# Kernel optimization log

Measured on AMD Instinct MI355X. Metric: run time of the kernel, lower is better.

Reference implementation:

```python
import jax, jax.numpy as jnp
import numpy as np

B, N, IN_C, HID, K1, K2, OUT_C = 128, 512, 128, 32, 100, 10, 10
E_PER = 8192  # edges per graph (avg degree 16)
EPS = 1e-15


def _lin(key, fan_in, fan_out):
    return jax.random.normal(key, (fan_in, fan_out), jnp.float32) / np.sqrt(fan_in)


def setup_inputs() -> dict:
    key = jax.random.key(0)
    ks = jax.random.split(key, 20)
    total = B * N
    x = jax.random.normal(ks[0], (total, IN_C), jnp.float32)
    # per-graph random edges, offset into the global node index space
    src_l = jax.random.randint(ks[1], (B, E_PER), 0, N)
    dst_l = jax.random.randint(ks[2], (B, E_PER), 0, N)
    off = (jnp.arange(B, dtype=jnp.int32) * N)[:, None]
    edge_index = jnp.stack([(src_l + off).reshape(-1), (dst_l + off).reshape(-1)]).astype(jnp.int32)
    batch = (jnp.arange(total, dtype=jnp.int32) // N).astype(jnp.int32)
    return {
        "x": x,
        "edge_index": edge_index,
        "batch": batch,
        "conv1_W": _lin(ks[3], IN_C, HID), "conv1_b": jnp.zeros((HID,), jnp.float32),
        "pool1_W": _lin(ks[4], HID, K1), "pool1_b": jnp.zeros((K1,), jnp.float32),
        "conv2_rel_W": _lin(ks[5], HID, HID), "conv2_rel_b": jnp.zeros((HID,), jnp.float32),
        "conv2_root_W": _lin(ks[6], HID, HID),
        "pool2_W": _lin(ks[7], HID, K2), "pool2_b": jnp.zeros((K2,), jnp.float32),
        "conv3_rel_W": _lin(ks[8], HID, HID), "conv3_rel_b": jnp.zeros((HID,), jnp.float32),
        "conv3_root_W": _lin(ks[9], HID, HID),
        "lin1_W": _lin(ks[10], HID, HID), "lin1_b": jnp.zeros((HID,), jnp.float32),
        "lin2_W": _lin(ks[11], HID, OUT_C), "lin2_b": jnp.zeros((OUT_C,), jnp.float32),
    }


def gcn_conv(x, edge_index, W, b):
    # GCNConv with add_self_loops=True, symmetric normalization
    total = x.shape[0]
    loops = jnp.arange(total, dtype=edge_index.dtype)
    src = jnp.concatenate([edge_index[0], loops])
    dst = jnp.concatenate([edge_index[1], loops])
    w = jnp.ones(src.shape[0], x.dtype)
    deg = jax.ops.segment_sum(w, dst, num_segments=total)
    dis = jnp.where(deg > 0, jax.lax.rsqrt(deg), 0.0)
    norm = dis[src] * dis[dst]
    xw = x @ W
    out = jax.ops.segment_sum(norm[:, None] * xw[src], dst, num_segments=total)
    return out + b


def dense_mincut_pool(x, adj, s, mask=None):
    # x:[b,n,f] adj:[b,n,n] s:[b,n,k]
    s = jax.nn.softmax(s, axis=-1)
    if mask is not None:
        m = mask[..., None].astype(x.dtype)
        x = x * m
        s = s * m
    out = jnp.einsum('bnk,bnf->bkf', s, x)
    out_adj = jnp.einsum('bnk,bnm,bml->bkl', s, adj, s)
    mincut_num = jnp.trace(out_adj, axis1=-2, axis2=-1)
    d_flat = adj.sum(-1)  # [b,n]
    mincut_den = jnp.einsum('bnk,bn,bnk->b', s, d_flat, s)  # trace(s^T D s)
    mincut_loss = jnp.mean(-(mincut_num / mincut_den))
    k = s.shape[-1]
    ss = jnp.einsum('bnk,bnl->bkl', s, s)
    ss_norm = jnp.linalg.norm(ss, axis=(-1, -2), keepdims=True)
    i_s = jnp.eye(k, dtype=x.dtype) / jnp.sqrt(jnp.asarray(k, x.dtype))  # I_k / ||I_k||_F
    ortho_loss = jnp.mean(jnp.linalg.norm(ss / ss_norm - i_s, axis=(-1, -2)))
    # zero diagonal then symmetric degree-normalize
    out_adj = out_adj * (1.0 - jnp.eye(k, dtype=x.dtype))
    d = jnp.sqrt(out_adj.sum(-1))[..., None] + EPS
    out_adj = out_adj / d / jnp.swapaxes(d, -1, -2)
    return out, out_adj, mincut_loss, ortho_loss


def dense_graph_conv(x, adj, rel_W, rel_b, root_W):
    # DenseGraphConv(aggr='add'): lin_rel(adj @ x) + lin_root(x)
    return (adj @ x) @ rel_W + rel_b + x @ root_W


def reference(x, edge_index, batch, conv1_W, conv1_b, pool1_W, pool1_b,
              conv2_rel_W, conv2_rel_b, conv2_root_W, pool2_W, pool2_b,
              conv3_rel_W, conv3_rel_b, conv3_root_W, lin1_W, lin1_b, lin2_W, lin2_b):
    h = jax.nn.relu(gcn_conv(x, edge_index, conv1_W, conv1_b))
    # to_dense_batch: sorted batch with N nodes per graph -> reshape; mask all-true
    xd = h.reshape(B, N, HID)
    mask = jnp.ones((B, N), bool)
    # to_dense_adj
    b_idx = edge_index[0] // N
    s_l = edge_index[0] % N
    d_l = edge_index[1] % N
    adj = jnp.zeros((B, N, N), x.dtype).at[b_idx, s_l, d_l].add(1.0)
    s = xd @ pool1_W + pool1_b
    xd, adj, mc1, o1 = dense_mincut_pool(xd, adj, s, mask)
    xd = jax.nn.relu(dense_graph_conv(xd, adj, conv2_rel_W, conv2_rel_b, conv2_root_W))
    s = xd @ pool2_W + pool2_b
    xd, adj, mc2, o2 = dense_mincut_pool(xd, adj, s)
    xd = dense_graph_conv(xd, adj, conv3_rel_W, conv3_rel_b, conv3_root_W)
    g = xd.mean(axis=1)  # [B, HID]
    g = jax.nn.relu(g @ lin1_W + lin1_b)
    g = g @ lin2_W + lin2_b
    return jax.nn.log_softmax(g, axis=-1), mc1 + mc2 + o1 + o2
```

## Files before the change

kernel.cpp:

```cpp
#include <hip/hip_runtime.h>
#include <hip/hip_bf16.h>

#define TB   128
#define NN   512
#define INC  128
#define HH   32
#define KP1  100
#define KP2  10
#define OC   10
#define EPER 8192
#define NT   (TB*NN)
#define ET   (TB*EPER)
#define ZTR  264
#define ZTS  40
#define XTS  136

typedef unsigned int  u32;
typedef unsigned short u16;
typedef __attribute__((ext_vector_type(8))) short bf16x8;
typedef __attribute__((ext_vector_type(16))) float f32x16;

__device__ __forceinline__ u32 bfr(float f) {
    u32 b = __float_as_uint(f);
    return (b + 0x7fffu + ((b >> 16) & 1u)) >> 16;
}
__device__ __forceinline__ u32 pk2(float a, float b) { return bfr(a) | (bfr(b) << 16); }
__device__ __forceinline__ float blo(u32 u) { return __uint_as_float(u << 16); }
__device__ __forceinline__ float bhi(u32 u) { return __uint_as_float(u & 0xffff0000u); }

__global__ __launch_bounds__(1024) void k_sort(const int* __restrict__ ei,
                                               int* __restrict__ cnt_src, int* __restrict__ cnt_dst,
                                               int* __restrict__ off_src, int* __restrict__ off_dst,
                                               u16* __restrict__ srt_dst, u16* __restrict__ srt_src,
                                               float* __restrict__ dis, float* __restrict__ aux) {
    __shared__ int hs[NN], hd[NN], ps[NN], pd[NN];
    __shared__ __align__(16) u16 sdl[EPER], ssl[EPER];
    int g = blockIdx.x, tid = threadIdx.x, goff = g * NN;
    if (tid == 0) aux[g] = 0.f;
    if (tid < NN) { hs[tid] = 0; hd[tid] = 0; }
    __syncthreads();
    const int* es = ei + (size_t)g * EPER;
    const int* ed = ei + ET + (size_t)g * EPER;
    for (int e = tid; e < EPER; e += 1024) {
        atomicAdd(&hs[es[e] - goff], 1);
        atomicAdd(&hd[ed[e] - goff], 1);
    }
    __syncthreads();
    int vs = 0, vd = 0;
    if (tid < NN) { vs = hs[tid]; vd = hd[tid]; ps[tid] = vs; pd[tid] = vd; }
    __syncthreads();
    for (int off = 1; off < NN; off <<= 1) {
        int xa = 0, xb = 0;
        if (tid < NN) {
            xa = ps[tid]; xb = pd[tid];
            if (tid >= off) { xa += ps[tid - off]; xb += pd[tid - off]; }
        }
        __syncthreads();
        if (tid < NN) { ps[tid] = xa; pd[tid] = xb; }
        __syncthreads();
    }
    int eso = 0, edo = 0;
    if (tid < NN) {
        eso = ps[tid] - vs; edo = pd[tid] - vd;
        cnt_src[goff + tid] = vs;  cnt_dst[goff + tid] = vd;
        off_src[goff + tid] = g * EPER + eso;
        off_dst[goff + tid] = g * EPER + edo;
        dis[goff + tid] = rsqrtf(1.0f + (float)vd);
    }
    __syncthreads();
    if (tid < NN) { ps[tid] = eso; pd[tid] = edo; }
    __syncthreads();
    for (int e = tid; e < EPER; e += 1024) {
        int s = es[e] - goff, d = ed[e] - goff;
        int p = atomicAdd(&ps[s], 1); sdl[p] = (u16)d;
        int q = atomicAdd(&pd[d], 1); ssl[q] = (u16)s;
    }
    __syncthreads();
    u32* wd = (u32*)(srt_dst + (size_t)g * EPER);
    u32* ws = (u32*)(srt_src + (size_t)g * EPER);
    const u32* rd = (const u32*)sdl;
    const u32* rs = (const u32*)ssl;
    for (int i = tid; i < EPER / 2; i += 1024) { wd[i] = rd[i]; ws[i] = rs[i]; }
}

__global__ __launch_bounds__(256) void k_xw2(const float* __restrict__ x, const float* __restrict__ W,
                                             u16* __restrict__ xwb) {
    __shared__ u16 sX[128 * XTS];
    __shared__ u16 sW[32 * XTS];
    int tid = threadIdx.x;
    int nbase = blockIdx.x * 128;
    for (int i = tid; i < INC * HH; i += 256) {
        int k = i >> 5, n = i & 31;
        sW[n * XTS + k] = (u16)bfr(W[i]);
    }
    for (int i = tid; i < 128 * 32; i += 256) {
        int r = i >> 5, q = i & 31;
        float4 v = ((const float4*)(x + (size_t)(nbase + r) * INC))[q];
        u32* dst = (u32*)&sX[r * XTS + q * 4];
        dst[0] = pk2(v.x, v.y);
        dst[1] = pk2(v.z, v.w);
    }
    __syncthreads();
    int wave = tid >> 6, lane = tid & 63;
    int lc = lane & 31, half = lane >> 5;
    f32x16 acc;
#pragma unroll
    for (int r = 0; r < 16; r++) acc[r] = 0.f;
#pragma unroll
    for (int kc = 0; kc < 8; kc++) {
        bf16x8 af  = *(const bf16x8*)&sX[(wave * 32 + lc) * XTS + kc * 16 + half * 8];
        bf16x8 bfv = *(const bf16x8*)&sW[lc * XTS + kc * 16 + half * 8];
        acc = __builtin_amdgcn_mfma_f32_32x32x16_bf16(af, bfv, acc, 0, 0, 0);
    }
#pragma unroll
    for (int r = 0; r < 16; r++) {
        int m = (r & 3) + 8 * (r >> 2) + 4 * half;
        int rowg = nbase + wave * 32 + m;
        xwb[(size_t)rowg * HH + lc] = (u16)bfr(acc[r]);
    }
}

__global__ __launch_bounds__(256) void k_gcng(const u16* __restrict__ ssrc, const int* __restrict__ od,
                                              const int* __restrict__ cd, const u32* __restrict__ xwb32,
                                              const float* __restrict__ dis, const float* __restrict__ bias,
                                              u32* __restrict__ hb32) {
    int tid = threadIdx.x;
    int b = blockIdx.x;
    int r8 = b & 7, j = b >> 3;
    int g = r8 + 8 * (j & 15);
    int chunk = j >> 4;
    int n = g * NN + chunk * 16 + (tid >> 4), cp = tid & 15;
    int goff = g * NN;
    int base = od[n], cnt = cd[n];
    float dn = dis[n];
    u32 us = xwb32[(size_t)n * 16 + cp];
    float a0 = dn * blo(us), a1 = dn * bhi(us);
    int i = 0;
    for (; i + 4 <= cnt; i += 4) {
        int s0 = goff + ssrc[base + i],     s1v = goff + ssrc[base + i + 1];
        int s2 = goff + ssrc[base + i + 2], s3  = goff + ssrc[base + i + 3];
        float d0 = dis[s0], d1 = dis[s1v], d2 = dis[s2], d3 = dis[s3];
        u32 u0 = xwb32[(size_t)s0 * 16 + cp];
        u32 u1 = xwb32[(size_t)s1v * 16 + cp];
        u32 u2 = xwb32[(size_t)s2 * 16 + cp];
        u32 u3 = xwb32[(size_t)s3 * 16 + cp];
        a0 += d0 * blo(u0) + d1 * blo(u1) + d2 * blo(u2) + d3 * blo(u3);
        a1 += d0 * bhi(u0) + d1 * bhi(u1) + d2 * bhi(u2) + d3 * bhi(u3);
    }
    for (; i < cnt; i++) {
        int s0 = goff + ssrc[base + i]; float d0 = dis[s0];
        u32 u0 = xwb32[(size_t)s0 * 16 + cp];
        a0 += d0 * blo(u0); a1 += d0 * bhi(u0);
    }
    float v0 = fmaxf(dn * a0 + bias[2 * cp], 0.f);
    float v1 = fmaxf(dn * a1 + bias[2 * cp + 1], 0.f);
    hb32[(size_t)n * 16 + cp] = pk2(v0, v1);
}

__global__ __launch_bounds__(256) void k_s1m(const u32* __restrict__ hb32, const float* __restrict__ W,
                                             const float* __restrict__ bias, const int* __restrict__ csrc,
                                             u16* __restrict__ s1b, float* __restrict__ den1) {
    __shared__ u16 sH[128 * ZTS];
    __shared__ u16 sW[128 * ZTS];
    int tid = threadIdx.x;
    int nbase = blockIdx.x * 128;
    for (int i = tid; i < HH * KP1; i += 256) {
        int k = i / KP1, n = i - k * KP1;
        sW[n * ZTS + k] = (u16)bfr(W[i]);
    }
    for (int i = tid; i < 28 * 16; i += 256) {
        int n = 100 + (i >> 4), q = i & 15;
        ((u32*)sW)[n * (ZTS / 2) + q] = 0;
    }
    for (int i = tid; i < 128 * 16; i += 256) {
        int r = i >> 4, q = i & 15;
        ((u32*)sH)[r * (ZTS / 2) + q] = hb32[(size_t)(nbase + r) * 16 + q];
    }
    __syncthreads();
    int wave = tid >> 6, lane = tid & 63;
    int lc = lane & 31, half = lane >> 5;
    f32x16 acc[4];
#pragma unroll
    for (int t = 0; t < 4; t++)
#pragma unroll
        for (int r = 0; r < 16; r++) acc[t][r] = 0.f;
#pragma unroll
    for (int kc = 0; kc < 2; kc++) {
        bf16x8 af = *(const bf16x8*)&sH[(wave * 32 + lc) * ZTS + kc * 16 + half * 8];
#pragma unroll
        for (int t = 0; t < 4; t++) {
            bf16x8 bfv = *(const bf16x8*)&sW[(t * 32 + lc) * ZTS + kc * 16 + half * 8];
            acc[t] = __builtin_amdgcn_mfma_f32_32x32x16_bf16(af, bfv, acc[t], 0, 0, 0);
        }
    }
    float s[16], q[16];
#pragma unroll
    for (int r = 0; r < 16; r++) { s[r] = 0.f; q[r] = 0.f; }
#pragma unroll
    for (int t = 0; t < 4; t++) {
        int ch = t * 32 + lc;
        bool valid = ch < KP1;
        float bv = valid ? bias[ch] : 0.f;
#pragma unroll
        for (int r = 0; r < 16; r++) {
            float ev = valid ? __expf(acc[t][r] + bv) : 0.f;
            acc[t][r] = ev; s[r] += ev; q[r] = fmaf(ev, ev, q[r]);
        }
    }
#pragma unroll
    for (int off = 16; off >= 1; off >>= 1) {
#pragma unroll
        for (int r = 0; r < 16; r++) { s[r] += __shfl_xor(s[r], off); q[r] += __shfl_xor(q[r], off); }
    }
    float inv[16];
#pragma unroll
    for (int r = 0; r < 16; r++) inv[r] = 1.f / s[r];
#pragma unroll
    for (int t = 0; t < 4; t++) {
        int ch = t * 32 + lc;
        if (ch < KP1) {
#pragma unroll
            for (int r = 0; r < 16; r++) {
                int lr = (r & 3) + 8 * (r >> 2) + 4 * half;
                int rowg = nbase + wave * 32 + lr;
                s1b[(size_t)rowg * KP1 + ch] = (u16)bfr(acc[t][r] * inv[r]);
            }
        }
    }
    float contrib = 0.f;
    if (lc == 0) {
#pragma unroll
        for (int r = 0; r < 16; r++) {
            int lr = (r & 3) + 8 * (r >> 2) + 4 * half;
            int rowg = nbase + wave * 32 + lr;
            contrib += (float)csrc[rowg] * q[r] * inv[r] * inv[r];
        }
    }
    contrib += __shfl_xor(contrib, 32);
    if (lane == 0) atomicAdd(&den1[nbase >> 9], contrib);
}

__global__ __launch_bounds__(256) void k_t1g(const u16* __restrict__ sdst, const int* __restrict__ osr,
                                             const int* __restrict__ csr, const u32* __restrict__ s1b32,
                                             u32* __restrict__ t1b32) {
    int tid = threadIdx.x;
    int b = blockIdx.x;
    int r8 = b & 7, j = b >> 3;
    int g = r8 + 8 * (j & 15);
    int chunk = j >> 4;
    int n = g * NN + chunk * 4 + (tid >> 6), lane = tid & 63;
    if (lane >= 50) return;
    int goff = g * NN;
    int base = osr[n], cnt = csr[n];
    float a0 = 0.f, a1 = 0.f;
    int i = 0;
    for (; i + 4 <= cnt; i += 4) {
        int d0 = goff + sdst[base + i],     d1 = goff + sdst[base + i + 1];
        int d2 = goff + sdst[base + i + 2], d3 = goff + sdst[base + i + 3];
        u32 u0 = s1b32[(size_t)d0 * 50 + lane];
        u32 u1 = s1b32[(size_t)d1 * 50 + lane];
        u32 u2 = s1b32[(size_t)d2 * 50 + lane];
        u32 u3 = s1b32[(size_t)d3 * 50 + lane];
        a0 += (blo(u0) + blo(u1)) + (blo(u2) + blo(u3));
        a1 += (bhi(u0) + bhi(u1)) + (bhi(u2) + bhi(u3));
    }
    for (; i < cnt; i++) {
        int d0 = goff + sdst[base + i];
        u32 u0 = s1b32[(size_t)d0 * 50 + lane];
        a0 += blo(u0); a1 += bhi(u0);
    }
    t1b32[(size_t)n * 50 + lane] = pk2(a0, a1);
}

__device__ __forceinline__ void ld_cp(const u32* __restrict__ sp, int rstr,
                                      u32& w0, u32& w1, u32& w2, u32& w3) {
    w0 = sp[0]; w1 = sp[rstr]; w2 = sp[2 * rstr]; w3 = sp[3 * rstr];
}
__device__ __forceinline__ void st_cp(u16* __restrict__ zb, int doff,
                                      u32 w0, u32 w1, u32 w2, u32 w3) {
    u32 lo01 = (w0 & 0xffffu) | (w1 << 16);
    u32 lo23 = (w2 & 0xffffu) | (w3 << 16);
    u32 hi01 = (w0 >> 16) | (w1 & 0xffff0000u);
    u32 hi23 = (w2 >> 16) | (w3 & 0xffff0000u);
    *(uint2*)&zb[doff]       = make_uint2(lo01, lo23);
    *(uint2*)&zb[doff + ZTS] = make_uint2(hi01, hi23);
}

#define GRAM_MFMA(zb)                                                                               \
    {                                                                                               \
        bf16x8 af0 = *(const bf16x8*)&(zb)[(132 + (2*mtb    )*32 + lc)*ZTS + mfh*16 + half*8];      \
        bf16x8 af1 = *(const bf16x8*)&(zb)[(132 + (2*mtb + 1)*32 + lc)*ZTS + mfh*16 + half*8];      \
        bf16x8 bv0 = *(const bf16x8*)&(zb)[((2*ctb    )*32 + lc)*ZTS + mfh*16 + half*8];            \
        bf16x8 bv1 = *(const bf16x8*)&(zb)[((2*ctb + 1)*32 + lc)*ZTS + mfh*16 + half*8];            \
        acc00 = __builtin_amdgcn_mfma_f32_32x32x16_bf16(af0, bv0, acc00, 0, 0, 0);                  \
        acc01 = __builtin_amdgcn_mfma_f32_32x32x16_bf16(af0, bv1, acc01, 0, 0, 0);                  \
        acc10 = __builtin_amdgcn_mfma_f32_32x32x16_bf16(af1, bv0, acc10, 0, 0, 0);                  \
        acc11 = __builtin_amdgcn_mfma_f32_32x32x16_bf16(af1, bv1, acc11, 0, 0, 0);                  \
    }

#define DUMP_TILE(AV, MT, CT, ADD)                                                                  \
    {                                                                                               \
        int l = (CT) * 32 + lc;                                                                     \
        if (l < 232) {                                                                              \
            _Pragma("unroll")                                                                       \
            for (int r = 0; r < 16; r++) {                                                          \
                int k = (MT) * 32 + (r & 3) + 8 * (r >> 2) + 4 * half;                              \
                if (k < KP1) {                                                                      \
                    if (ADD) sC[k * 232 + l] += AV[r];                                              \
                    else     sC[k * 232 + l] = AV[r];                                               \
                }                                                                                   \
            }                                                                                       \
        }                                                                                           \
    }

__global__ __launch_bounds__(1024, 1) void k_gram(const u32* __restrict__ s1b32, const u32* __restrict__ t1b32,
                                                  const u32* __restrict__ hb32,
                                                  float* __restrict__ A1n, float* __restrict__ P1,
                                                  float* __restrict__ aux) {
    __shared__ __align__(16) u16 sZ[2][ZTR * ZTS];
    __shared__ float sC[KP1 * 232];
    __shared__ float sRow[KP1], sd[KP1];
    __shared__ float sScal[3];
    int g = blockIdx.x;
    int nbase = g * NN;
    int tid = threadIdx.x;
    int wave = tid >> 6, lane = tid & 63;
    int mfh = wave & 1;
    int mtb = (wave >> 1) & 1;
    int ctb = wave >> 2;
    int lc = lane & 31, half = lane >> 5;

    f32x16 acc00, acc01, acc10, acc11;
#pragma unroll
    for (int r = 0; r < 16; r++) { acc00[r] = 0.f; acc01[r] = 0.f; acc10[r] = 0.f; acc11[r] = 0.f; }

    int cp = (tid & 7) + ((tid >> 6) << 3);
    int rq = (tid >> 3) & 7;
    bool act = cp < 116;
    const u32* sp;
    int rstr;
    if (cp < 50)      { sp = t1b32 + cp;        rstr = 50; }
    else if (cp < 66) { sp = hb32 + (cp - 50);  rstr = 16; }
    else              { sp = s1b32 + (cp - 66); rstr = 50; }
    sp += (size_t)(nbase + rq * 4) * rstr;
    int step = rstr * 32;
    int doff = (2 * cp) * ZTS + rq * 4;

    if (tid < KP1) sRow[tid] = 0.f;
    if (tid < 3) sScal[tid] = 0.f;
    for (int i = tid; i < 32 * ZTS; i += 1024) {
        int r = 232 + i / ZTS, c = i % ZTS;
        sZ[0][r * ZTS + c] = 0; sZ[1][r * ZTS + c] = 0;
    }
    u32 a0, a1, a2, a3, b0 = 0, b1 = 0, b2 = 0, b3 = 0;
    if (act) {
        ld_cp(sp, rstr, a0, a1, a2, a3);
        st_cp(sZ[0], doff, a0, a1, a2, a3);
        sp += step;
        ld_cp(sp, rstr, b0, b1, b2, b3);
        sp += step;
    }
    __syncthreads();

    for (int nt = 0; nt < 16; nt += 2) {
        GRAM_MFMA(sZ[0]);
        if (act) {
            st_cp(sZ[1], doff, b0, b1, b2, b3);
            if (nt + 2 < 16) { ld_cp(sp, rstr, a0, a1, a2, a3); sp += step; }
        }
        __syncthreads();
        GRAM_MFMA(sZ[1]);
        if (act && nt + 2 < 16) {
            st_cp(sZ[0], doff, a0, a1, a2, a3);
            if (nt + 3 < 16) { ld_cp(sp, rstr, b0, b1, b2, b3); sp += step; }
        }
        __syncthreads();
    }
    if (mfh == 0) {
        DUMP_TILE(acc00, 2 * mtb,     2 * ctb,     0)
        DUMP_TILE(acc01, 2 * mtb,     2 * ctb + 1, 0)
        DUMP_TILE(acc10, 2 * mtb + 1, 2 * ctb,     0)
        DUMP_TILE(acc11, 2 * mtb + 1, 2 * ctb + 1, 0)
    }
    __syncthreads();
    if (mfh == 1) {
        DUMP_TILE(acc00, 2 * mtb,     2 * ctb,     1)
        DUMP_TILE(acc01, 2 * mtb,     2 * ctb + 1, 1)
        DUMP_TILE(acc10, 2 * mtb + 1, 2 * ctb,     1)
        DUMP_TILE(acc11, 2 * mtb + 1, 2 * ctb + 1, 1)
    }
    __syncthreads();
    float ssq = 0.f, trss = 0.f, troa = 0.f;
    for (int idx = tid; idx < KP1 * 58; idx += 1024) {
        int k = idx / 58, q = idx - k * 58;
        float4 s = *(const float4*)&sC[k * 232 + q * 4];
        int c = q * 4;
        if (c < 100) {
            float rs = (s.x + s.y) + (s.z + s.w);
            if (k >= c && k < c + 4) { float d = ((const float*)&s)[k - c]; troa += d; rs -= d; }
            atomicAdd(&sRow[k], rs);
        } else if (c < 132) {
            *(float4*)&P1[((size_t)g * KP1 + k) * HH + (c - 100)] = s;
        } else {
            ssq += s.x * s.x + s.y * s.y + s.z * s.z + s.w * s.w;
            int l0 = c - 132;
            if (k >= l0 && k < l0 + 4) trss += ((const float*)&s)[k - l0];
        }
    }
#pragma unroll
    for (int off = 32; off >= 1; off >>= 1) {
        ssq  += __shfl_xor(ssq, off);
        trss += __shfl_xor(trss, off);
        troa += __shfl_xor(troa, off);
    }
    if ((tid & 63) == 0) {
        atomicAdd(&sScal[0], troa);
        atomicAdd(&sScal[1], trss);
        atomicAdd(&sScal[2], ssq);
    }
    __syncthreads();
    if (tid == 0) {
        float o1 = sqrtf(fmaxf(2.f - 2.f * sScal[1] / (sqrtf(sScal[2]) * 10.f), 0.f));
        aux[128 + g] = -(sScal[0] / aux[g]) + o1;
    }
    if (tid < KP1) sd[tid] = sqrtf(sRow[tid]) + 1e-15f;
    __syncthreads();
    for (int i = tid; i < KP1 * KP1; i += 1024) {
        int k = i / KP1, l = i - k * KP1;
        A1n[(size_t)g * (KP1 * KP1) + i] = (k == l) ? 0.f : sC[k * 232 + l] / (sd[k] * sd[l]);
    }
}

__global__ __launch_bounds__(512) void k_s2(const float* __restrict__ A1n, const float* __restrict__ P1,
                                            const float* __restrict__ relW, const float* __restrict__ relB,
                                            const float* __restrict__ rootW,
                                            const float* __restrict__ p2W, const float* __restrict__ p2B,
                                            const float* __restrict__ relW3, const float* __restrict__ relb3,
                                            const float* __restrict__ rootW3,
                                            const float* __restrict__ l1W, const float* __restrict__ l1b,
                                            const float* __restrict__ l2W, const float* __restrict__ l2b,
                                            float* __restrict__ out, float* __restrict__ aux) {
    __shared__ float sA[KP1 * KP1];
    __shared__ float sX[KP1 * HH];
    __shared__ float sY[KP1 * HH];
    __shared__ float sS2[KP1 * KP2];
    __shared__ float sT2[KP1 * KP2];
    __shared__ float sA2[100], sB2[100], sdd[10], red[100];
    __shared__ float sP2[KP2 * HH], sAn[100], sY3[KP2 * HH], sG[32], sG1[32], sL[10], sLse;
    int g = blockIdx.x, tid = threadIdx.x;
    const float* Ag = A1n + (size_t)g * (KP1 * KP1);
    for (int i = tid; i < KP1 * KP1 / 4; i += 512)
        ((float4*)sA)[i] = ((const float4*)Ag)[i];
    for (int i = tid; i < KP1 * HH; i += 512) sX[i] = P1[(size_t)g * (KP1 * HH) + i];
    if (tid < 32) sG[tid] = 0.f;
    __syncthreads();

    int n = tid >> 2, cq = tid & 3;
    if (tid < 400) {
        float yv[8];
#pragma unroll
        for (int j = 0; j < 8; j++) yv[j] = 0.f;
        for (int mq = 0; mq < 25; mq++) {
            float4 a4 = *(const float4*)&sA[n * KP1 + mq * 4];
            const float* xb = &sX[(mq * 4) * HH + cq * 8];
            float aa[4] = {a4.x, a4.y, a4.z, a4.w};
#pragma unroll
            for (int mm = 0; mm < 4; mm++) {
                const float* xr = xb + mm * HH;
#pragma unroll
                for (int j = 0; j < 8; j++) yv[j] = fmaf(aa[mm], xr[j], yv[j]);
            }
        }
#pragma unroll
        for (int j = 0; j < 8; j++) sY[n * HH + cq * 8 + j] = yv[j];
    }
    __syncthreads();
    float x2v[8];
    if (tid < 400) {
#pragma unroll
        for (int j = 0; j < 8; j++) x2v[j] = relB[cq * 8 + j];
        for (int j = 0; j < 32; j++) {
            float yj = sY[n * HH + j];
            float xj = sX[n * HH + j];
            float4 r0 = *(const float4*)&relW[j * 32 + cq * 8];
            float4 r1v = *(const float4*)&relW[j * 32 + cq * 8 + 4];
            float4 q0 = *(const float4*)&rootW[j * 32 + cq * 8];
            float4 q1 = *(const float4*)&rootW[j * 32 + cq * 8 + 4];
            x2v[0] += yj * r0.x + xj * q0.x;  x2v[1] += yj * r0.y + xj * q0.y;
            x2v[2] += yj * r0.z + xj * q0.z;  x2v[3] += yj * r0.w + xj * q0.w;
            x2v[4] += yj * r1v.x + xj * q1.x; x2v[5] += yj * r1v.y + xj * q1.y;
            x2v[6] += yj * r1v.z + xj * q1.z; x2v[7] += yj * r1v.w + xj * q1.w;
        }
    }
    __syncthreads();
    if (tid < 400) {
#pragma unroll
        for (int j = 0; j < 8; j++) sX[n * HH + cq * 8 + j] = fmaxf(x2v[j], 0.f);
    }
    __syncthreads();
    if (tid < KP1) {
        float lg[10];
#pragma unroll
        for (int j = 0; j < 10; j++) lg[j] = p2B[j];
        for (int c = 0; c < 32; c++) {
            float xv = sX[tid * HH + c];
#pragma unroll
            for (int j = 0; j < 10; j++) lg[j] = fmaf(xv, p2W[c * 10 + j], lg[j]);
        }
        float mx = lg[0];
#pragma unroll
        for (int j = 1; j < 10; j++) mx = fmaxf(mx, lg[j]);
        float se = 0.f;
#pragma unroll
        for (int j = 0; j < 10; j++) { lg[j] = __expf(lg[j] - mx); se += lg[j]; }
        float inv = 1.f / se, sq = 0.f;
#pragma unroll
        for (int j = 0; j < 10; j++) { float sv = lg[j] * inv; sS2[tid * 10 + j] = sv; sq += sv * sv; }
        float d2 = 0.f;
        for (int mq = 0; mq < 25; mq++) {
            float4 a4 = *(const float4*)&sA[tid * KP1 + mq * 4];
            d2 += a4.x + a4.y + a4.z + a4.w;
        }
        red[tid] = d2 * sq;
    }
    __syncthreads();
    for (int p = tid; p < KP1 * KP2; p += 512) {
        int n2 = p / 10, jj = p % 10;
        float a = 0.f;
        for (int m = 0; m < KP1; m++) a = fmaf(sA[n2 * KP1 + m], sS2[m * 10 + jj], a);
        sT2[p] = a;
    }
    if (tid < KP2 * HH) {
        int k = tid >> 5, cc = tid & 31;
        float a = 0.f;
        for (int n2 = 0; n2 < KP1; n2++) a = fmaf(sS2[n2 * 10 + k], sX[n2 * HH + cc], a);
        sP2[tid] = a;
    }
    __syncthreads();
    if (tid < 100) {
        int k = tid / 10, l = tid % 10;
        float oa = 0.f, ss = 0.f;
        for (int n2 = 0; n2 < KP1; n2++) {
            float sk = sS2[n2 * 10 + k];
            oa = fmaf(sk, sT2[n2 * 10 + l], oa);
            ss = fmaf(sk, sS2[n2 * 10 + l], ss);
        }
        sA2[tid] = oa; sB2[tid] = ss;
    }
    __syncthreads();
    if (tid == 0) {
        float den2 = 0.f;
        for (int i = 0; i < 100; i++) den2 += red[i];
        float troa = 0.f, trss = 0.f, ssq = 0.f;
        for (int k = 0; k < 10; k++) { troa += sA2[k * 10 + k]; trss += sB2[k * 10 + k]; }
        for (int i = 0; i < 100; i++) ssq += sB2[i] * sB2[i];
        float o2 = sqrtf(fmaxf(2.f - 2.f * trss / (sqrtf(ssq) * 3.16227766f), 0.f));
        aux[256 + g] = -(troa / den2) + o2;
    }
    if (tid < 10) {
        float rs = 0.f;
        for (int l = 0; l < 10; l++) if (l != tid) rs += sA2[tid * 10 + l];
        sdd[tid] = sqrtf(rs) + 1e-15f;
    }
    __syncthreads();
    if (tid < 100) {
        int k = tid / 10, l = tid % 10;
        sAn[tid] = (k == l) ? 0.f : sA2[tid] / (sdd[k] * sdd[l]);
    }
    __syncthreads();
    if (tid < KP2 * HH) {
        int k = tid >> 5, cc = tid & 31;
        float a = 0.f;
#pragma unroll
        for (int m = 0; m < 10; m++) a = fmaf(sAn[k * 10 + m], sP2[m * HH + cc], a);
        sY3[tid] = a;
    }
    __syncthreads();
    if (tid < KP2 * HH) {
        int k = tid >> 5, cc = tid & 31;
        float v = relb3[cc];
        for (int j = 0; j < 32; j++)
            v += sY3[k * HH + j] * relW3[j * 32 + cc] + sP2[k * HH + j] * rootW3[j * 32 + cc];
        atomicAdd(&sG[cc], v * 0.1f);
    }
    __syncthreads();
    if (tid < 32) {
        float v = l1b[tid];
        for (int j = 0; j < 32; j++) v = fmaf(sG[j], l1W[j * 32 + tid], v);
        sG1[tid] = fmaxf(v, 0.f);
    }
    __syncthreads();
    if (tid < 10) {
        float v = l2b[tid];
        for (int j = 0; j < 32; j++) v = fmaf(sG1[j], l2W[j * 10 + tid], v);
        sL[tid] = v;
    }
    __syncthreads();
    if (tid == 0) {
        float mx = sL[0];
        for (int j = 1; j < 10; j++) mx = fmaxf(mx, sL[j]);
        float se = 0.f;
        for (int j = 0; j < 10; j++) se += expf(sL[j] - mx);
        sLse = mx + logf(se);
    }
    __syncthreads();
    if (tid < 10) out[(size_t)g * 10 + tid] = sL[tid] - sLse;
}

__global__ void k_loss(const float* __restrict__ aux, float* __restrict__ out) {
    __shared__ float red[128];
    int tid = threadIdx.x;
    red[tid] = aux[128 + tid] + aux[256 + tid];
    __syncthreads();
#pragma unroll
    for (int s = 64; s > 0; s >>= 1) { if (tid < s) red[tid] += red[tid + s]; __syncthreads(); }
    if (tid == 0) out[1280] = red[0] * (1.f / 128.f);
}

extern "C" void kernel_launch(void* const* d_in, const int* in_sizes, int n_in,
                              void* d_out, int out_size, void* d_ws, size_t ws_size,
                              hipStream_t stream) {
    const float* x    = (const float*)d_in[0];
    const int*   ei   = (const int*)d_in[1];
    const float* c1W  = (const float*)d_in[3];
    const float* c1b  = (const float*)d_in[4];
    const float* p1W  = (const float*)d_in[5];
    const float* p1b  = (const float*)d_in[6];
    const float* relW2  = (const float*)d_in[7];
    const float* relb2  = (const float*)d_in[8];
    const float* rootW2 = (const float*)d_in[9];
    const float* p2W  = (const float*)d_in[10];
    const float* p2b  = (const float*)d_in[11];
    const float* relW3  = (const float*)d_in[12];
    const float* relb3  = (const float*)d_in[13];
    const float* rootW3 = (const float*)d_in[14];
    const float* l1W  = (const float*)d_in[15];
    const float* l1b  = (const float*)d_in[16];
    const float* l2W  = (const float*)d_in[17];
    const float* l2b  = (const float*)d_in[18];
    float* out = (float*)d_out;

    int*  cnt_src = (int*)d_ws;
    int*  cnt_dst = cnt_src + NT;
    int*  off_src = cnt_dst + NT;
    int*  off_dst = off_src + NT;
    u16*  srt_dst = (u16*)(off_dst + NT);
    u16*  srt_src = srt_dst + ET;
    float* dis = (float*)(srt_src + ET);
    u32*  xwb  = (u32*)(dis + NT);
    u32*  hb   = xwb + (size_t)NT * 16;
    u32*  s1b  = hb + (size_t)NT * 16;
    u32*  t1b  = s1b + (size_t)NT * 50;
    float* A1n  = (float*)(t1b + (size_t)NT * 50);
    float* P1   = A1n + (size_t)TB * KP1 * KP1;
    float* aux  = P1 + (size_t)TB * KP1 * HH;

    k_sort<<<TB, 1024, 0, stream>>>(ei, cnt_src, cnt_dst, off_src, off_dst, srt_dst, srt_src, dis, aux);
    k_xw2<<<NT / 128, 256, 0, stream>>>(x, c1W, (u16*)xwb);
    k_gcng<<<NT / 16, 256, 0, stream>>>(srt_src, off_dst, cnt_dst, xwb, dis, c1b, hb);
    k_s1m<<<NT / 128, 256, 0, stream>>>(hb, p1W, p1b, cnt_src, (u16*)s1b, aux );
    k_t1g<<<NT / 4, 256, 0, stream>>>(srt_dst, off_src, cnt_src, s1b, t1b);
    k_gram<<<TB, 1024, 0, stream>>>(s1b, t1b, hb, A1n, P1, aux);
    k_s2<<<TB, 512, 0, stream>>>(A1n, P1, relW2, relb2, rootW2, p2W, p2b,
                                 relW3, relb3, rootW3, l1W, l1b, l2W, l2b, out, aux);
    k_loss<<<1, 128, 0, stream>>>(aux, out);
}
```

Before: 250.1 us.

## Fuse edge sort with XW, merge gram with pool2 stage, drop loss kernel

Merges the edge-sort kernel and the x@W projection into one launch: the first 128 blocks do the CSR sort and the rest each project 512 nodes. The gram kernel now runs the second pooling, convs and head in place on its shared-memory tile, so the A1n/P1 round trip through global memory and the k_s2 launch go away. The final loss reduction becomes an atomicAdd into the output, removing the k_loss launch. Trade-offs are larger shared-memory use per block, 1024-thread blocks on the small dense stage with only 128 blocks, and a float atomic order that is non-deterministic.

Result: no change. 248.4 us (-0.7%).

```diff
diff --git a/kernel.cpp b/kernel.cpp
--- a/kernel.cpp
+++ b/kernel.cpp
@@ -28,72 +28,78 @@
 __device__ __forceinline__ float blo(u32 u) { return __uint_as_float(u << 16); }
 __device__ __forceinline__ float bhi(u32 u) { return __uint_as_float(u & 0xffff0000u); }
 
-__global__ __launch_bounds__(1024) void k_sort(const int* __restrict__ ei,
-                                               int* __restrict__ cnt_src, int* __restrict__ cnt_dst,
-                                               int* __restrict__ off_src, int* __restrict__ off_dst,
-                                               u16* __restrict__ srt_dst, u16* __restrict__ srt_src,
-                                               float* __restrict__ dis, float* __restrict__ aux) {
-    __shared__ int hs[NN], hd[NN], ps[NN], pd[NN];
-    __shared__ __align__(16) u16 sdl[EPER], ssl[EPER];
-    int g = blockIdx.x, tid = threadIdx.x, goff = g * NN;
-    if (tid == 0) aux[g] = 0.f;
-    if (tid < NN) { hs[tid] = 0; hd[tid] = 0; }
-    __syncthreads();
-    const int* es = ei + (size_t)g * EPER;
-    const int* ed = ei + ET + (size_t)g * EPER;
-    for (int e = tid; e < EPER; e += 1024) {
-        atomicAdd(&hs[es[e] - goff], 1);
-        atomicAdd(&hd[ed[e] - goff], 1);
-    }
-    __syncthreads();
-    int vs = 0, vd = 0;
-    if (tid < NN) { vs = hs[tid]; vd = hd[tid]; ps[tid] = vs; pd[tid] = vd; }
-    __syncthreads();
-    for (int off = 1; off < NN; off <<= 1) {
-        int xa = 0, xb = 0;
+__global__ __launch_bounds__(1024) void k_pre(const int* __restrict__ ei,
+                                              int* __restrict__ cnt_src, int* __restrict__ cnt_dst,
+                                              int* __restrict__ off_src, int* __restrict__ off_dst,
+                                              u16* __restrict__ srt_dst, u16* __restrict__ srt_src,
+                                              float* __restrict__ dis, float* __restrict__ aux,
+                                              const float* __restrict__ x, const float* __restrict__ W,
+                                              u16* __restrict__ xwb, float* __restrict__ out) {
+    __shared__ __align__(16) u16 sX[512 * XTS];
+    __shared__ __align__(16) u16 sW[32 * XTS];
+    int tid = threadIdx.x, b = blockIdx.x;
+    if (b < TB) {
+        int* hs = (int*)sX;
+        int* hd = hs + NN;
+        int* ps = hd + NN;
+        int* pd = ps + NN;
+        u16* sdl = (u16*)(pd + NN);
+        u16* ssl = sdl + EPER;
+        int g = b, goff = g * NN;
+        if (tid == 0) aux[g] = 0.f;
+        if (g == 0 && tid == 0) out[1280] = 0.f;
+        if (tid < NN) { hs[tid] = 0; hd[tid] = 0; }
+        __syncthreads();
+        const int* es = ei + (size_t)g * EPER;
+        const int* ed = ei + ET + (size_t)g * EPER;
+        for (int e = tid; e < EPER; e += 1024) {
+            atomicAdd(&hs[es[e] - goff], 1);
+            atomicAdd(&hd[ed[e] - goff], 1);
+        }
+        __syncthreads();
+        int vs = 0, vd = 0;
+        if (tid < NN) { vs = hs[tid]; vd = hd[tid]; ps[tid] = vs; pd[tid] = vd; }
+        __syncthreads();
+        for (int off = 1; off < NN; off <<= 1) {
+            int xa = 0, xb = 0;
+            if (tid < NN) {
+                xa = ps[tid]; xb = pd[tid];
+                if (tid >= off) { xa += ps[tid - off]; xb += pd[tid - off]; }
+            }
+            __syncthreads();
+            if (tid < NN) { ps[tid] = xa; pd[tid] = xb; }
+            __syncthreads();
+        }
+        int eso = 0, edo = 0;
         if (tid < NN) {
-            xa = ps[tid]; xb = pd[tid];
-            if (tid >= off) { xa += ps[tid - off]; xb += pd[tid - off]; }
-        }
-        __syncthreads();
-        if (tid < NN) { ps[tid] = xa; pd[tid] = xb; }
-        __syncthreads();
-    }
-    int eso = 0, edo = 0;
-    if (tid < NN) {
-        eso = ps[tid] - vs; edo = pd[tid] - vd;
-        cnt_src[goff + tid] = vs;  cnt_dst[goff + tid] = vd;
-        off_src[goff + tid] = g * EPER + eso;
-        off_dst[goff + tid] = g * EPER + edo;
-        dis[goff + tid] = rsqrtf(1.0f + (float)vd);
-    }
-    __syncthreads();
-    if (tid < NN) { ps[tid] = eso; pd[tid] = edo; }
-    __syncthreads();
-    for (int e = tid; e < EPER; e += 1024) {
-        int s = es[e] - goff, d = ed[e] - goff;
-        int p = atomicAdd(&ps[s], 1); sdl[p] = (u16)d;
-        int q = atomicAdd(&pd[d], 1); ssl[q] = (u16)s;
-    }
-    __syncthreads();
-    u32* wd = (u32*)(srt_dst + (size_t)g * EPER);
-    u32* ws = (u32*)(srt_src + (size_t)g * EPER);
-    const u32* rd = (const u32*)sdl;
-    const u32* rs = (const u32*)ssl;
-    for (int i = tid; i < EPER / 2; i += 1024) { wd[i] = rd[i]; ws[i] = rs[i]; }
-}
-
-__global__ __launch_bounds__(256) void k_xw2(const float* __restrict__ x, const float* __restrict__ W,
-                                             u16* __restrict__ xwb) {
-    __shared__ u16 sX[128 * XTS];
-    __shared__ u16 sW[32 * XTS];
-    int tid = threadIdx.x;
-    int nbase = blockIdx.x * 128;
-    for (int i = tid; i < INC * HH; i += 256) {
+            eso = ps[tid] - vs; edo = pd[tid] - vd;
+            cnt_src[goff + tid] = vs;  cnt_dst[goff + tid] = vd;
+            off_src[goff + tid] = g * EPER + eso;
+            off_dst[goff + tid] = g * EPER + edo;
+            dis[goff + tid] = rsqrtf(1.0f + (float)vd);
+        }
+        __syncthreads();
+        if (tid < NN) { ps[tid] = eso; pd[tid] = edo; }
+        __syncthreads();
+        for (int e = tid; e < EPER; e += 1024) {
+            int s = es[e] - goff, d = ed[e] - goff;
+            int p = atomicAdd(&ps[s], 1); sdl[p] = (u16)d;
+            int q = atomicAdd(&pd[d], 1); ssl[q] = (u16)s;
+        }
+        __syncthreads();
+        u32* wd = (u32*)(srt_dst + (size_t)g * EPER);
+        u32* ws = (u32*)(srt_src + (size_t)g * EPER);
+        const u32* rd = (const u32*)sdl;
+        const u32* rs = (const u32*)ssl;
+        for (int i = tid; i < EPER / 2; i += 1024) { wd[i] = rd[i]; ws[i] = rs[i]; }
+        return;
+    }
+    int nbase = (b - TB) * 512;
+    for (int i = tid; i < INC * HH; i += 1024) {
         int k = i >> 5, n = i & 31;
         sW[n * XTS + k] = (u16)bfr(W[i]);
     }
-    for (int i = tid; i < 128 * 32; i += 256) {
+    for (int i = tid; i < 512 * 32; i += 1024) {
         int r = i >> 5, q = i & 31;
         float4 v = ((const float4*)(x + (size_t)(nbase + r) * INC))[q];
         u32* dst = (u32*)&sX[r * XTS + q * 4];
@@ -313,14 +319,21 @@
         }                                                                                           \
     }
 
-__global__ __launch_bounds__(1024, 1) void k_gram(const u32* __restrict__ s1b32, const u32* __restrict__ t1b32,
-                                                  const u32* __restrict__ hb32,
-                                                  float* __restrict__ A1n, float* __restrict__ P1,
-                                                  float* __restrict__ aux) {
+__global__ __launch_bounds__(1024, 1) void k_gram2(const u32* __restrict__ s1b32, const u32* __restrict__ t1b32,
+                                                   const u32* __restrict__ hb32, const float* __restrict__ aux,
+                                                   const float* __restrict__ relW, const float* __restrict__ relB,
+                                                   const float* __restrict__ rootW,
+                                                   const float* __restrict__ p2W, const float* __restrict__ p2B,
+                                                   const float* __restrict__ relW3, const float* __restrict__ relb3,
+                                                   const float* __restrict__ rootW3,
+                                                   const float* __restrict__ l1W, const float* __restrict__ l1b,
+                                                   const float* __restrict__ l2W, const float* __restrict__ l2b,
+                                                   float* __restrict__ out) {
     __shared__ __align__(16) u16 sZ[2][ZTR * ZTS];
     __shared__ float sC[KP1 * 232];
     __shared__ float sRow[KP1], sd[KP1];
     __shared__ float sScal[3];
+    __shared__ float sL1;
     int g = blockIdx.x;
     int nbase = g * NN;
     int tid = threadIdx.x;
@@ -329,6 +342,23 @@
     int mtb = (wave >> 1) & 1;
     int ctb = wave >> 2;
     int lc = lane & 31, half = lane >> 5;
+
+    float* ov  = (float*)sZ;
+    float* sXo = ov;
+    float* sYo = ov + 3200;
+    float* sS2 = ov + 6400;
+    float* sT2 = ov + 7400;
+    float* sA2 = ov + 8400;
+    float* sB2 = ov + 8500;
+    float* red = ov + 8600;
+    float* sP2 = ov + 8700;
+    float* sY3 = ov + 9020;
+    float* sAn = ov + 9340;
+    float* sG  = ov + 9440;
+    float* sG1 = ov + 9472;
+    float* sL  = ov + 9504;
+    float* sdd = ov + 9514;
+    float* sLse = ov + 9524;
 
     f32x16 acc00, acc01, acc10, acc11;
 #pragma unroll
@@ -390,68 +420,50 @@
         DUMP_TILE(acc11, 2 * mtb + 1, 2 * ctb + 1, 1)
     }
     __syncthreads();
-    float ssq = 0.f, trss = 0.f, troa = 0.f;
-    for (int idx = tid; idx < KP1 * 58; idx += 1024) {
-        int k = idx / 58, q = idx - k * 58;
-        float4 s = *(const float4*)&sC[k * 232 + q * 4];
-        int c = q * 4;
-        if (c < 100) {
-            float rs = (s.x + s.y) + (s.z + s.w);
-            if (k >= c && k < c + 4) { float d = ((const float*)&s)[k - c]; troa += d; rs -= d; }
-            atomicAdd(&sRow[k], rs);
-        } else if (c < 132) {
-            *(float4*)&P1[((size_t)g * KP1 + k) * HH + (c - 100)] = s;
-        } else {
-            ssq += s.x * s.x + s.y * s.y + s.z * s.z + s.w * s.w;
-            int l0 = c - 132;
-            if (k >= l0 && k < l0 + 4) trss += ((const float*)&s)[k - l0];
-        }
-    }
-#pragma unroll
-    for (int off = 32; off >= 1; off >>= 1) {
-        ssq  += __shfl_xor(ssq, off);
-        trss += __shfl_xor(trss, off);
-        troa += __shfl_xor(troa, off);
-    }
-    if ((tid & 63) == 0) {
-        atomicAdd(&sScal[0], troa);
-        atomicAdd(&sScal[1], trss);
-        atomicAdd(&sScal[2], ssq);
+    {
+        float ssq = 0.f, trss = 0.f, troa = 0.f;
+        for (int idx = tid; idx < KP1 * 58; idx += 1024) {
+            int k = idx / 58, q = idx - k * 58;
+            float4 s = *(const float4*)&sC[k * 232 + q * 4];
+            int c = q * 4;
+            if (c < 100) {
+                float rs = (s.x + s.y) + (s.z + s.w);
+                if (k >= c && k < c + 4) { float d = ((const float*)&s)[k - c]; troa += d; rs -= d; }
+                atomicAdd(&sRow[k], rs);
+            } else if (c >= 132) {
+                ssq += s.x * s.x + s.y * s.y + s.z * s.z + s.w * s.w;
+                int l0 = c - 132;
+                if (k >= l0 && k < l0 + 4) trss += ((const float*)&s)[k - l0];
+            }
+        }
+#pragma unroll
+        for (int off = 32; off >= 1; off >>= 1) {
+            ssq  += __shfl_xor(ssq, off);
+            trss += __shfl_xor(trss, off);
+            troa += __shfl_xor(troa, off);
+        }
+        if ((tid & 63) == 0) {
+            atomicAdd(&sScal[0], troa);
+            atomicAdd(&sScal[1], trss);
+            atomicAdd(&sScal[2], ssq);
+        }
     }
     __syncthreads();
     if (tid == 0) {
         float o1 = sqrtf(fmaxf(2.f - 2.f * sScal[1] / (sqrtf(sScal[2]) * 10.f), 0.f));
-        aux[128 + g] = -(sScal[0] / aux[g]) + o1;
+        sL1 = -(sScal[0] / aux[g]) + o1;
     }
     if (tid < KP1) sd[tid] = sqrtf(sRow[tid]) + 1e-15f;
     __syncthreads();
     for (int i = tid; i < KP1 * KP1; i += 1024) {
         int k = i / KP1, l = i - k * KP1;
-        A1n[(size_t)g * (KP1 * KP1) + i] = (k == l) ? 0.f : sC[k * 232 + l] / (sd[k] * sd[l]);
-    }
-}
-
-__global__ __launch_bounds__(512) void k_s2(const float* __restrict__ A1n, const float* __restrict__ P1,
-                                            const float* __restrict__ relW, const float* __restrict__ relB,
-                                            const float* __restrict__ rootW,
-                                            const float* __restrict__ p2W, const float* __restrict__ p2B,
-                                            const float* __restrict__ relW3, const float* __restrict__ relb3,
-                                            const float* __restrict__ rootW3,
-                                            const float* __restrict__ l1W, const float* __restrict__ l1b,
-                                            const float* __restrict__ l2W, const float* __restrict__ l2b,
-                                            float* __restrict__ out, float* __restrict__ aux) {
-    __shared__ float sA[KP1 * KP1];
-    __shared__ float sX[KP1 * HH];
-    __shared__ float sY[KP1 * HH];
-    __shared__ float sS2[KP1 * KP2];
-    __shared__ float sT2[KP1 * KP2];
-    __shared__ float sA2[100], sB2[100], sdd[10], red[100];
-    __shared__ float sP2[KP2 * HH], sAn[100], sY3[KP2 * HH], sG[32], sG1[32], sL[10], sLse;
-    int g = blockIdx.x, tid = threadIdx.x;
-    const float* Ag = A1n + (size_t)g * (KP1 * KP1);
-    for (int i = tid; i < KP1 * KP1 / 4; i += 512)
-        ((float4*)sA)[i] = ((const float4*)Ag)[i];
-    for (int i = tid; i < KP1 * HH; i += 512) sX[i] = P1[(size_t)g * (KP1 * HH) + i];
+        float v = sC[k * 232 + l];
+        sC[k * 232 + l] = (k == l) ? 0.f : v / (sd[k] * sd[l]);
+    }
+    for (int i = tid; i < KP1 * HH; i += 1024) {
+        int k = i >> 5, c = i & 31;
+        sXo[i] = sC[k * 232 + 100 + c];
+    }
     if (tid < 32) sG[tid] = 0.f;
     __syncthreads();
 
@@ -461,8 +473,8 @@
 #pragma unroll
         for (int j = 0; j < 8; j++) yv[j] = 0.f;
         for (int mq = 0; mq < 25; mq++) {
-            float4 a4 = *(const float4*)&sA[n * KP1 + mq * 4];
-            const float* xb = &sX[(mq * 4) * HH + cq * 8];
+            float4 a4 = *(const float4*)&sC[n * 232 + mq * 4];
+            const float* xb = &sXo[(mq * 4) * HH + cq * 8];
             float aa[4] = {a4.x, a4.y, a4.z, a4.w};
 #pragma unroll
             for (int mm = 0; mm < 4; mm++) {
@@ -472,7 +484,7 @@
             }
         }
 #pragma unroll
-        for (int j = 0; j < 8; j++) sY[n * HH + cq * 8 + j] = yv[j];
+        for (int j = 0; j < 8; j++) sYo[n * HH + cq * 8 + j] = yv[j];
     }
     __syncthreads();
     float x2v[8];
@@ -480,8 +492,8 @@
 #pragma unroll
         for (int j = 0; j < 8; j++) x2v[j] = relB[cq * 8 + j];
         for (int j = 0; j < 32; j++) {
-            float yj = sY[n * HH + j];
-            float xj = sX[n * HH + j];
+            float yj = sYo[n * HH + j];
+            float xj = sXo[n * HH + j];
             float4 r0 = *(const float4*)&relW[j * 32 + cq * 8];
             float4 r1v = *(const float4*)&relW[j * 32 + cq * 8 + 4];
             float4 q0 = *(const float4*)&rootW[j * 32 + cq * 8];
@@ -495,7 +507,7 @@
     __syncthreads();
     if (tid < 400) {
 #pragma unroll
-        for (int j = 0; j < 8; j++) sX[n * HH + cq * 8 + j] = fmaxf(x2v[j], 0.f);
+        for (int j = 0; j < 8; j++) sXo[n * HH + cq * 8 + j] = fmaxf(x2v[j], 0.f);
     }
     __syncthreads();
     if (tid < KP1) {
@@ -503,7 +515,7 @@
 #pragma unroll
         for (int j = 0; j < 10; j++) lg[j] = p2B[j];
         for (int c = 0; c < 32; c++) {
-            float xv = sX[tid * HH + c];
+            float xv = sXo[tid * HH + c];
 #pragma unroll
             for (int j = 0; j < 10; j++) lg[j] = fmaf(xv, p2W[c * 10 + j], lg[j]);
         }
@@ -518,22 +530,22 @@
         for (int j = 0; j < 10; j++) { float sv = lg[j] * inv; sS2[tid * 10 + j] = sv; sq += sv * sv; }
         float d2 = 0.f;
         for (int mq = 0; mq < 25; mq++) {
-            float4 a4 = *(const float4*)&sA[tid * KP1 + mq * 4];
+            float4 a4 = *(const float4*)&sC[tid * 232 + mq * 4];
             d2 += a4.x + a4.y + a4.z + a4.w;
         }
         red[tid] = d2 * sq;
     }
     __syncthreads();
-    for (int p = tid; p < KP1 * KP2; p += 512) {
+    for (int p = tid; p < KP1 * KP2; p += 1024) {
         int n2 = p / 10, jj = p % 10;
         float a = 0.f;
-        for (int m = 0; m < KP1; m++) a = fmaf(sA[n2 * KP1 + m], sS2[m * 10 + jj], a);
+        for (int m = 0; m < KP1; m++) a = fmaf(sC[n2 * 232 + m], sS2[m * 10 + jj], a);
         sT2[p] = a;
     }
     if (tid < KP2 * HH) {
         int k = tid >> 5, cc = tid & 31;
         float a = 0.f;
-        for (int n2 = 0; n2 < KP1; n2++) a = fmaf(sS2[n2 * 10 + k], sX[n2 * HH + cc], a);
+        for (int n2 = 0; n2 < KP1; n2++) a = fmaf(sS2[n2 * 10 + k], sXo[n2 * HH + cc], a);
         sP2[tid] = a;
     }
     __syncthreads();
@@ -555,7 +567,8 @@
         for (int k = 0; k < 10; k++) { troa += sA2[k * 10 + k]; trss += sB2[k * 10 + k]; }
         for (int i = 0; i < 100; i++) ssq += sB2[i] * sB2[i];
         float o2 = sqrtf(fmaxf(2.f - 2.f * trss / (sqrtf(ssq) * 3.16227766f), 0.f));
-        aux[256 + g] = -(troa / den2) + o2;
+        float l2 = -(troa / den2) + o2;
+        atomicAdd(&out[1280], (sL1 + l2) * (1.f / 128.f));
     }
     if (tid < 10) {
         float rs = 0.f;
@@ -601,20 +614,10 @@
         for (int j = 1; j < 10; j++) mx = fmaxf(mx, sL[j]);
         float se = 0.f;
         for (int j = 0; j < 10; j++) se += expf(sL[j] - mx);
-        sLse = mx + logf(se);
-    }
-    __syncthreads();
-    if (tid < 10) out[(size_t)g * 10 + tid] = sL[tid] - sLse;
-}
-
-__global__ void k_loss(const float* __restrict__ aux, float* __restrict__ out) {
-    __shared__ float red[128];
-    int tid = threadIdx.x;
-    red[tid] = aux[128 + tid] + aux[256 + tid];
-    __syncthreads();
-#pragma unroll
-    for (int s = 64; s > 0; s >>= 1) { if (tid < s) red[tid] += red[tid + s]; __syncthreads(); }
-    if (tid == 0) out[1280] = red[0] * (1.f / 128.f);
+        *sLse = mx + logf(se);
+    }
+    __syncthreads();
+    if (tid < 10) out[(size_t)g * 10 + tid] = sL[tid] - *sLse;
 }
 
 extern "C" void kernel_launch(void* const* d_in, const int* in_sizes, int n_in,
@@ -651,17 +654,13 @@
     u32*  hb   = xwb + (size_t)NT * 16;
     u32*  s1b  = hb + (size_t)NT * 16;
     u32*  t1b  = s1b + (size_t)NT * 50;
-    float* A1n  = (float*)(t1b + (size_t)NT * 50);
-    float* P1   = A1n + (size_t)TB * KP1 * KP1;
-    float* aux  = P1 + (size_t)TB * KP1 * HH;
-
-    k_sort<<<TB, 1024, 0, stream>>>(ei, cnt_src, cnt_dst, off_src, off_dst, srt_dst, srt_src, dis, aux);
-    k_xw2<<<NT / 128, 256, 0, stream>>>(x, c1W, (u16*)xwb);
+    float* aux  = (float*)(t1b + (size_t)NT * 50);
+
+    k_pre<<<2 * TB, 1024, 0, stream>>>(ei, cnt_src, cnt_dst, off_src, off_dst,
+                                       srt_dst, srt_src, dis, aux, x, c1W, (u16*)xwb, out);
     k_gcng<<<NT / 16, 256, 0, stream>>>(srt_src, off_dst, cnt_dst, xwb, dis, c1b, hb);
     k_s1m<<<NT / 128, 256, 0, stream>>>(hb, p1W, p1b, cnt_src, (u16*)s1b, aux );
     k_t1g<<<NT / 4, 256, 0, stream>>>(srt_dst, off_src, cnt_src, s1b, t1b);
-    k_gram<<<TB, 1024, 0, stream>>>(s1b, t1b, hb, A1n, P1, aux);
-    k_s2<<<TB, 512, 0, stream>>>(A1n, P1, relW2, relb2, rootW2, p2W, p2b,
-                                 relW3, relb3, rootW3, l1W, l1b, l2W, l2b, out, aux);
-    k_loss<<<1, 128, 0, stream>>>(aux, out);
-}
+    k_gram2<<<TB, 1024, 0, stream>>>(s1b, t1b, hb, aux, relW2, relb2, rootW2, p2W, p2b,
+                                     relW3, relb3, rootW3, l1W, l1b, l2W, l2b, out);
+}
```
